# Optimization experiments

Measured on AMD Instinct MI355X. Metric: run time of the kernel, lower is better.

The kernel has to match this reference:

```python
import jax, jax.numpy as jnp
import numpy as np

DIMVEC = 196
POS_LABEL = 98
NBLABELS = 10
M = 128
UNIHIGH = 0.012
BATCH = 8192


def setup_inputs() -> dict:
    key = jax.random.key(0)
    ks = jax.random.split(key, 6)
    # input features: one 2-vector per site, normalized to unit norm (cos/sin style)
    x = jax.random.uniform(ks[0], (BATCH, DIMVEC, 2), dtype=jnp.float32)
    x = x / jnp.linalg.norm(x, axis=-1, keepdims=True)
    # MPS tensors, uniform(0, unihigh) as in the original construct_tensornetwork
    w0 = jax.random.uniform(ks[1], (2, M), dtype=jnp.float32) * UNIHIGH
    w_left = jax.random.uniform(ks[2], (POS_LABEL - 1, 2, M, M), dtype=jnp.float32) * UNIHIGH
    w_label = jax.random.uniform(ks[3], (2, M, M, NBLABELS), dtype=jnp.float32) * UNIHIGH
    w_right = jax.random.uniform(ks[4], (DIMVEC - 2 - POS_LABEL, 2, M, M), dtype=jnp.float32) * UNIHIGH
    w_end = jax.random.uniform(ks[5], (2, M), dtype=jnp.float32) * UNIHIGH
    return {"x": x, "w0": w0, "w_left": w_left, "w_label": w_label,
            "w_right": w_right, "w_end": w_end}


def reference(x, w0, w_left, w_label, w_right, w_end):
    b, d, _ = x.shape
    m = w0.shape[1]

    # left boundary: contract physical leg of site 0 -> [B, m]
    left = x[:, 0, :] @ w0

    # sweep sites 1 .. pos_label-1: left'[b,n] = sum_{p,mm} x[b,p] left[b,mm] W[p,mm,n]
    def lstep(carry, inp):
        W, xi = inp                       # W: [2,m,m], xi: [B,2]
        o = (xi[:, :, None] * carry[:, None, :]).reshape(b, 2 * m)  # [B, 2m]
        return o @ W.reshape(2 * m, m), None                        # GEMM B x 2m x m

    left, _ = jax.lax.scan(lstep, left,
                           (w_left, jnp.swapaxes(x[:, 1:POS_LABEL], 0, 1)))

    # right boundary: contract physical leg of last site -> [B, m]
    right = x[:, -1, :] @ w_end

    # sweep sites dimvec-2 .. pos_label+1 (reverse):
    # right'[b,mm] = sum_{p,n} x[b,p] right[b,n] W[p,mm,n]
    def rstep(carry, inp):
        W, xi = inp
        o = (xi[:, :, None] * carry[:, None, :]).reshape(b, 2 * m)  # [B, 2m]
        Wt = jnp.swapaxes(W, 1, 2).reshape(2 * m, m)                # [p,n,mm] -> [2m, m]
        return o @ Wt, None

    right, _ = jax.lax.scan(rstep, right,
                            (w_right, jnp.swapaxes(x[:, POS_LABEL + 1:d - 1], 0, 1)),
                            reverse=True)

    # label site: contract left bond first (small intermediate [B,2,m,L])
    xl = x[:, POS_LABEL, :]                                   # [B, 2]
    z = jnp.einsum('bm,pmnl->bpnl', left, w_label)             # [B,2,m,L]
    leftL = jnp.einsum('bpnl,bp->bnl', z, xl)                  # [B,m,L]

    # close the chain with the right environment -> [B, nblabels]
    return jnp.einsum('bnl,bn->bl', leftL, right)
```

## Files before the change

kernel.cpp:

```cpp
#include <hip/hip_runtime.h>

#define BATCH 8192
#define MDIM 128
#define NL 10
#define LSTEPS 97
#define RSTEPS 96
#define NSTEPS 193
#define DIM 196
#define POSL 98

typedef _Float16 half8 __attribute__((ext_vector_type(8)));
typedef float float16v __attribute__((ext_vector_type(16)));

#define BARRIER_LGKM() asm volatile("s_waitcnt lgkmcnt(0)\ns_barrier" ::: "memory")

#define MFMA16 __builtin_amdgcn_mfma_f32_32x32x16_f16

__global__ __launch_bounds__(256) void transpose_x(const float* __restrict__ x,
                                                   float2* __restrict__ xT) {
    __shared__ float tx[64][65];
    __shared__ float ty[64][65];
    int p0 = blockIdx.x * 32;
    int b0 = blockIdx.y * 64;
    int tid = threadIdx.x;

    int r = tid >> 2, q = tid & 3;
    const float* src = x + ((size_t)(b0 + r) * DIM + p0 + q * 8) * 2;
#pragma unroll
    for (int j = 0; j < 8; ++j) {
        int pp = q * 8 + j;
        if (p0 + pp < DIM) {
            float2 v = *(const float2*)(src + j * 2);
            tx[r][pp] = v.x;
            ty[r][pp] = v.y;
        }
    }
    __syncthreads();

    int pr = tid >> 3, cb = (tid & 7) * 8;
    if (p0 + pr < DIM) {
        float2* dst = xT + (size_t)(p0 + pr) * BATCH + b0 + cb;
#pragma unroll
        for (int j = 0; j < 8; ++j) {
            float2 v;
            v.x = tx[cb + j][pr];
            v.y = ty[cb + j][pr];
            dst[j] = v;
        }
    }
}

__global__ __launch_bounds__(256) void pack_w(const float* __restrict__ w_left,
                                              const float* __restrict__ w_right,
                                              _Float16* __restrict__ pw) {
    int g = blockIdx.x >> 2;
    int nt = blockIdx.x & 3;
    int tid = threadIdx.x;
    int l = tid & 63;
    int kq = tid >> 6;
    int hi = l >> 5;
    int n = nt * 32 + (l & 31);
#pragma unroll
    for (int p = 0; p < 4; ++p) {
        int kt = p * 4 + kq;
        int k0 = kt * 16 + hi * 8;
        half8 hv;
        if (g < LSTEPS) {
            const float* base = w_left + (size_t)g * 2 * MDIM * MDIM;
#pragma unroll
            for (int j = 0; j < 8; ++j)
                hv[j] = (_Float16)base[(size_t)(k0 + j) * MDIM + n];
        } else {
            int t = g - LSTEPS;
            int s = k0 >> 7;
            int a0 = k0 & 127;
            const float* row = w_right + (size_t)(RSTEPS - 1 - t) * 2 * MDIM * MDIM
                             + (size_t)s * MDIM * MDIM + (size_t)n * MDIM + a0;
#pragma unroll
            for (int j = 0; j < 8; ++j) hv[j] = (_Float16)row[j];
        }
        *(half8*)(pw + (size_t)(g * 64 + nt * 16 + kt) * 512 + l * 8) = hv;
    }
}

__global__ __launch_bounds__(256) void pack_label(const float* __restrict__ w_label,
                                                  _Float16* __restrict__ gp) {
    int ct = blockIdx.x;
    int tid = threadIdx.x;
    int l = tid & 63;
    int kq = tid >> 6;
    int hi = l >> 5;
    int outcol = ct * 32 + (l & 31);
    int n = outcol & 127;
    int lab = outcol >> 7;
#pragma unroll
    for (int p2 = 0; p2 < 4; ++p2) {
        int kt = p2 * 4 + kq;
        int k0 = kt * 16 + hi * 8;
        int p = k0 >> 7;
        int m0 = k0 & 127;
        half8 hv;
#pragma unroll
        for (int j = 0; j < 8; ++j)
            hv[j] = (_Float16)w_label[(((size_t)p * MDIM + m0 + j) * MDIM + n) * NL + lab];
        *(half8*)(gp + (size_t)(ct * 16 + kt) * 512 + l * 8) = hv;
    }
}


#define LD16(dst, p, ofs) \
    asm volatile("global_load_dwordx4 %0, %1, off offset:" ofs : "=v"(dst) : "v"(p))

#define ISSUE_A(DST, PN) do {                                  \
    const char* _p0 = (PN);                                    \
    LD16(DST[0],  _p0, "0");                                   \
    LD16(DST[1],  _p0, "1024");                                \
    LD16(DST[2],  _p0, "2048");                                \
    LD16(DST[3],  _p0, "3072");                                \
    const char* _p1 = _p0 + 4096;                              \
    LD16(DST[4],  _p1, "0");                                   \
    LD16(DST[5],  _p1, "1024");                                \
    LD16(DST[6],  _p1, "2048");                                \
    LD16(DST[7],  _p1, "3072");                                \
    const char* _p2 = _p0 + 8192;                              \
    LD16(DST[8],  _p2, "0");                                   \
    LD16(DST[9],  _p2, "1024");                                \
    LD16(DST[10], _p2, "2048");                                \
    LD16(DST[11], _p2, "3072");                                \
    const char* _p3 = _p0 + 12288;                             \
    LD16(DST[12], _p3, "0");                                   \
    LD16(DST[13], _p3, "1024");                                \
    LD16(DST[14], _p3, "2048");                                \
    LD16(DST[15], _p3, "3072");                                \
} while (0)

#define WAIT_A16() do {                                        \
    asm volatile("s_waitcnt vmcnt(16)" ::: "memory");          \
    __builtin_amdgcn_sched_barrier(0);                         \
} while (0)

#define WAIT_A0() do {                                         \
    asm volatile("s_waitcnt vmcnt(0)" ::: "memory");           \
    __builtin_amdgcn_sched_barrier(0);                         \
} while (0)

#define CHAIN_MFMA_BLOCK(AF, SRC)                                            \
    half8 bf0[8], bf1[8];                                                    \
    _Pragma("unroll")                                                        \
    for (int q = 0; q < 8; ++q) {                                            \
        int nb = q * 2 + hi;                                                 \
        int phys = nb ^ (bl & 15);                                           \
        bf0[q] = *(const half8*)&cbuf[SRC][bl * 128 + phys * 8];             \
        bf1[q] = *(const half8*)&cbuf[SRC][(bl + 32) * 128 + phys * 8];      \
    }                                                                        \
    float16v a00 = {}, a01 = {}, a10 = {}, a11 = {};                         \
    _Pragma("unroll")                                                        \
    for (int kt = 0; kt < 8; ++kt) {                                         \
        a00 = MFMA16(AF[kt], bf0[kt], a00, 0, 0, 0);                         \
        a10 = MFMA16(AF[kt], bf1[kt], a10, 0, 0, 0);                         \
        a01 = MFMA16(AF[kt + 8], bf0[kt], a01, 0, 0, 0);                     \
        a11 = MFMA16(AF[kt + 8], bf1[kt], a11, 0, 0, 0);                     \
    }

#define EPI_RG(DST, XC, A_LO, A_HI, ROWOFF)                                  \
    _Pragma("unroll")                                                        \
    for (int rq = 0; rq < 4; ++rq) {                                         \
        int nb = nt * 4 + rq;                                                \
        int phys = nb ^ (bl & 15);                                           \
        union { _Float16 h[4]; uint2 u; } t;                                 \
        _Pragma("unroll")                                                    \
        for (int r = 0; r < 4; ++r)                                          \
            t.h[r] = (_Float16)((XC).x * A_LO[rq * 4 + r]                    \
                              + (XC).y * A_HI[rq * 4 + r]);                  \
        *(uint2*)&cbuf[DST][(bl + ROWOFF) * 128 + phys * 8 + hi * 4] = t.u;  \
    }

#define FINAL_STORE()                                                        \
    _Pragma("unroll")                                                        \
    for (int r = 0; r < 16; ++r) {                                           \
        int n = nt * 32 + (r & 3) + 8 * (r >> 2) + 4 * hi;                   \
        outT[(size_t)n * BATCH + bbase + bl] = xc0.x * a00[r] + xc0.y * a01[r]; \
        outT[(size_t)n * BATCH + bbase + 32 + bl] = xc1.x * a10[r] + xc1.y * a11[r]; \
    }

__global__ __launch_bounds__(256, 1) void chain_mfma(
        const float2* __restrict__ xT, const float* __restrict__ w0,
        const float* __restrict__ w_end, const _Float16* __restrict__ pw,
        float* __restrict__ leftT, float* __restrict__ rightT) {
    __shared__ _Float16 cbuf[2][64 * 128];
    __shared__ float2 xbuf[98][64];

    int bid = blockIdx.x;
    bool is_left = bid < 128;
    int bbase = (is_left ? bid : bid - 128) * 64;
    int tid = threadIdx.x;
    int l = tid & 63;
    int nt = tid >> 6;
    int bl = l & 31;
    int hi = l >> 5;

    int nsteps = is_left ? LSTEPS : RSTEPS;
    int gbase = is_left ? 0 : LSTEPS;
    int pbase = is_left ? 0 : 98;
    float* outT = is_left ? leftT : rightT;

    for (int i = tid; i < 98 * 64; i += 256) {
        int pos = i >> 6, b = i & 63;
        xbuf[pos][b] = xT[(size_t)(pbase + pos) * BATCH + bbase + b];
    }
    __syncthreads();

    {
        const float* wst = is_left ? w0 : w_end;
        int b = tid >> 2;
        float2 xv0 = xbuf[is_left ? 0 : 97][b];
#pragma unroll
        for (int h = 0; h < 4; ++h) {
            int nb = (tid & 3) * 4 + h;
            half8 hv;
#pragma unroll
            for (int j = 0; j < 8; ++j) {
                int n = nb * 8 + j;
                hv[j] = (_Float16)(xv0.x * wst[n] + xv0.y * wst[MDIM + n]);
            }
            int phys = nb ^ (b & 15);
            *(half8*)&cbuf[0][b * 128 + phys * 8] = hv;
        }
    }

    const char* pwb = (const char*)pw + (size_t)(gbase * 64 + nt * 16) * 1024
                    + (size_t)l * 16;

    __syncthreads();

    half8 A0[16], A1[16];
    ISSUE_A(A0, pwb);

    int npairs = nsteps >> 1;
    bool oddtail = nsteps & 1;
    int last = nsteps - 1;

#pragma unroll 1
    for (int sp = 0; sp < npairs; ++sp) {
        int s0 = 2 * sp;
        {
            ISSUE_A(A1, pwb + (size_t)(s0 + 1) * 65536);
            WAIT_A16();
            int xi = is_left ? (1 + s0) : (96 - s0);
            float2 xc0 = xbuf[xi][bl];
            float2 xc1 = xbuf[xi][32 + bl];
            CHAIN_MFMA_BLOCK(A0, 0)
            EPI_RG(1, xc0, a00, a01, 0)
            EPI_RG(1, xc1, a10, a11, 32)
            BARRIER_LGKM();
        }
        {
            int s1 = s0 + 1;
            int pf = (s0 + 2 <= last) ? (s0 + 2) : last;
            ISSUE_A(A0, pwb + (size_t)pf * 65536);
            WAIT_A16();
            int xi = is_left ? (1 + s1) : (96 - s1);
            float2 xc0 = xbuf[xi][bl];
            float2 xc1 = xbuf[xi][32 + bl];
            CHAIN_MFMA_BLOCK(A1, 1)
            if (s1 == last) {
                FINAL_STORE()
            } else {
                EPI_RG(0, xc0, a00, a01, 0)
                EPI_RG(0, xc1, a10, a11, 32)
                BARRIER_LGKM();
            }
        }
    }

    if (oddtail) {
        WAIT_A0();
        int xi = 1 + last;
        float2 xc0 = xbuf[xi][bl];
        float2 xc1 = xbuf[xi][32 + bl];
        CHAIN_MFMA_BLOCK(A0, 0)
        FINAL_STORE()
    }
}

__global__ __launch_bounds__(256, 2) void label_mfma(
        const float2* __restrict__ xT, const _Float16* __restrict__ gp,
        const float* __restrict__ leftT, const float* __restrict__ rightT,
        float* __restrict__ out) {
    __shared__ _Float16 R[32 * 256];
    __shared__ float pl[4][32][5];
    __shared__ float xl_s[32][2];

    int bx = blockIdx.x;
    int bbase = blockIdx.y * 32;
    int tid = threadIdx.x;
    int l = tid & 63, nt = tid >> 6, bl = l & 31, hi = l >> 5;

    if (tid < 32) {
        const float2 v = xT[(size_t)POSL * BATCH + bbase + tid];
        xl_s[tid][0] = v.x; xl_s[tid][1] = v.y;
    }
    __syncthreads();

#pragma unroll
    for (int q = 0; q < 4; ++q) {
        int id = tid + q * 256;
        int m = id >> 3;
        int b4 = (id & 7) * 4;
        float4 v = *(const float4*)&leftT[(size_t)m * BATCH + bbase + b4];
        float vv[4] = {v.x, v.y, v.z, v.w};
#pragma unroll
        for (int bi = 0; bi < 4; ++bi) {
            int b = b4 + bi;
            int kb0 = m >> 3;
            int ph0 = (kb0 & 16) | ((kb0 ^ b) & 15);
            R[b * 256 + ph0 * 8 + (m & 7)] = (_Float16)(xl_s[b][0] * vv[bi]);
            int kb1 = kb0 + 16;
            int ph1 = (kb1 & 16) | ((kb1 ^ b) & 15);
            R[b * 256 + ph1 * 8 + (m & 7)] = (_Float16)(xl_s[b][1] * vv[bi]);
        }
    }

    float rv[16];
#pragma unroll
    for (int r = 0; r < 16; ++r) {
        int n = nt * 32 + (r & 3) + 8 * (r >> 2) + 4 * hi;
        rv[r] = rightT[(size_t)n * BATCH + bbase + bl];
    }
    __syncthreads();

    half8 rf[16];
#pragma unroll
    for (int kt = 0; kt < 16; ++kt) {
        int kb = kt * 2 + hi;
        int ph = (kb & 16) | ((kb ^ bl) & 15);
        rf[kt] = *(const half8*)&R[bl * 256 + ph * 8];
    }

    int l0 = bx * 5;
    float outv[5];
#pragma unroll
    for (int li = 0; li < 5; ++li) {
        int ct = (l0 + li) * 4 + nt;
        float16v acc = {};
#pragma unroll
        for (int kt = 0; kt < 16; ++kt) {
            half8 a = *(const half8*)(gp + (size_t)(ct * 16 + kt) * 512 + l * 8);
            acc = __builtin_amdgcn_mfma_f32_32x32x16_f16(a, rf[kt], acc, 0, 0, 0);
        }
        float p = 0.f;
#pragma unroll
        for (int r = 0; r < 16; ++r) p += acc[r] * rv[r];
        p += __shfl_xor(p, 32, 64);
        outv[li] = p;
    }
    if (hi == 0) {
#pragma unroll
        for (int li = 0; li < 5; ++li) pl[nt][bl][li] = outv[li];
    }
    __syncthreads();
    if (tid < 160) {
        int b = tid / 5, li = tid % 5;
        out[(size_t)(bbase + b) * NL + l0 + li] =
            pl[0][b][li] + pl[1][b][li] + pl[2][b][li] + pl[3][b][li];
    }
}

extern "C" void kernel_launch(void* const* d_in, const int* in_sizes, int n_in,
                              void* d_out, int out_size, void* d_ws, size_t ws_size,
                              hipStream_t stream) {
    const float* x       = (const float*)d_in[0];
    const float* w0      = (const float*)d_in[1];
    const float* w_left  = (const float*)d_in[2];
    const float* w_label = (const float*)d_in[3];
    const float* w_right = (const float*)d_in[4];
    const float* w_end   = (const float*)d_in[5];

    _Float16* pw = (_Float16*)d_ws;
    _Float16* gp = pw + (size_t)NSTEPS * 64 * 512;
    float* leftT  = (float*)(gp + (size_t)40 * 16 * 512);
    float* rightT = leftT + (size_t)MDIM * BATCH;
    float2* xT    = (float2*)(rightT + (size_t)MDIM * BATCH);

    transpose_x<<<dim3((DIM + 31) / 32, BATCH / 64), 256, 0, stream>>>(x, xT);
    pack_w<<<dim3(NSTEPS * 4), 256, 0, stream>>>(w_left, w_right, pw);
    pack_label<<<dim3(40), 256, 0, stream>>>(w_label, gp);
    chain_mfma<<<dim3(256), 256, 0, stream>>>(xT, w0, w_end, pw, leftT, rightT);
    label_mfma<<<dim3(2, BATCH / 32), 256, 0, stream>>>(xT, gp, leftT, rightT,
                                                        (float*)d_out);
}
```

Before: 241.8 us.

## Split chain kernel batch rows across two wave groups with 512-thread blocks

```diff
diff --git a/kernel.cpp b/kernel.cpp
--- a/kernel.cpp
+++ b/kernel.cpp
@@ -145,24 +145,21 @@
 } while (0)
 
 #define CHAIN_MFMA_BLOCK(AF, SRC)                                            \
-    half8 bf0[8], bf1[8];                                                    \
+    half8 bf[8];                                                             \
     _Pragma("unroll")                                                        \
     for (int q = 0; q < 8; ++q) {                                            \
         int nb = q * 2 + hi;                                                 \
         int phys = nb ^ (bl & 15);                                           \
-        bf0[q] = *(const half8*)&cbuf[SRC][bl * 128 + phys * 8];             \
-        bf1[q] = *(const half8*)&cbuf[SRC][(bl + 32) * 128 + phys * 8];      \
+        bf[q] = *(const half8*)&cbuf[SRC][row * 128 + phys * 8];             \
     }                                                                        \
-    float16v a00 = {}, a01 = {}, a10 = {}, a11 = {};                         \
+    float16v a0 = {}, a1 = {};                                               \
     _Pragma("unroll")                                                        \
     for (int kt = 0; kt < 8; ++kt) {                                         \
-        a00 = MFMA16(AF[kt], bf0[kt], a00, 0, 0, 0);                         \
-        a10 = MFMA16(AF[kt], bf1[kt], a10, 0, 0, 0);                         \
-        a01 = MFMA16(AF[kt + 8], bf0[kt], a01, 0, 0, 0);                     \
-        a11 = MFMA16(AF[kt + 8], bf1[kt], a11, 0, 0, 0);                     \
-    }
-
-#define EPI_RG(DST, XC, A_LO, A_HI, ROWOFF)                                  \
+        a0 = MFMA16(AF[kt], bf[kt], a0, 0, 0, 0);                            \
+        a1 = MFMA16(AF[kt + 8], bf[kt], a1, 0, 0, 0);                        \
+    }
+
+#define EPI_RG(DST, XC)                                                      \
     _Pragma("unroll")                                                        \
     for (int rq = 0; rq < 4; ++rq) {                                         \
         int nb = nt * 4 + rq;                                                \
@@ -170,20 +167,19 @@
         union { _Float16 h[4]; uint2 u; } t;                                 \
         _Pragma("unroll")                                                    \
         for (int r = 0; r < 4; ++r)                                          \
-            t.h[r] = (_Float16)((XC).x * A_LO[rq * 4 + r]                    \
-                              + (XC).y * A_HI[rq * 4 + r]);                  \
-        *(uint2*)&cbuf[DST][(bl + ROWOFF) * 128 + phys * 8 + hi * 4] = t.u;  \
-    }
-
-#define FINAL_STORE()                                                        \
+            t.h[r] = (_Float16)((XC).x * a0[rq * 4 + r]                      \
+                              + (XC).y * a1[rq * 4 + r]);                    \
+        *(uint2*)&cbuf[DST][row * 128 + phys * 8 + hi * 4] = t.u;            \
+    }
+
+#define FINAL_STORE(XC)                                                      \
     _Pragma("unroll")                                                        \
     for (int r = 0; r < 16; ++r) {                                           \
         int n = nt * 32 + (r & 3) + 8 * (r >> 2) + 4 * hi;                   \
-        outT[(size_t)n * BATCH + bbase + bl] = xc0.x * a00[r] + xc0.y * a01[r]; \
-        outT[(size_t)n * BATCH + bbase + 32 + bl] = xc1.x * a10[r] + xc1.y * a11[r]; \
-    }
-
-__global__ __launch_bounds__(256, 1) void chain_mfma(
+        outT[(size_t)n * BATCH + bbase + row] = (XC).x * a0[r] + (XC).y * a1[r]; \
+    }
+
+__global__ __launch_bounds__(512, 2) void chain_mfma(
         const float2* __restrict__ xT, const float* __restrict__ w0,
         const float* __restrict__ w_end, const _Float16* __restrict__ pw,
         float* __restrict__ leftT, float* __restrict__ rightT) {
@@ -195,16 +191,19 @@
     int bbase = (is_left ? bid : bid - 128) * 64;
     int tid = threadIdx.x;
     int l = tid & 63;
-    int nt = tid >> 6;
+    int w = tid >> 6;
+    int nt = w & 3;
+    int rg = w >> 2;
     int bl = l & 31;
     int hi = l >> 5;
+    int row = rg * 32 + bl;
 
     int nsteps = is_left ? LSTEPS : RSTEPS;
     int gbase = is_left ? 0 : LSTEPS;
     int pbase = is_left ? 0 : 98;
     float* outT = is_left ? leftT : rightT;
 
-    for (int i = tid; i < 98 * 64; i += 256) {
+    for (int i = tid; i < 98 * 64; i += 512) {
         int pos = i >> 6, b = i & 63;
         xbuf[pos][b] = xT[(size_t)(pbase + pos) * BATCH + bbase + b];
     }
@@ -212,11 +211,11 @@
 
     {
         const float* wst = is_left ? w0 : w_end;
-        int b = tid >> 2;
+        int b = tid >> 3;
         float2 xv0 = xbuf[is_left ? 0 : 97][b];
 #pragma unroll
-        for (int h = 0; h < 4; ++h) {
-            int nb = (tid & 3) * 4 + h;
+        for (int h = 0; h < 2; ++h) {
+            int nb = (tid & 7) * 2 + h;
             half8 hv;
 #pragma unroll
             for (int j = 0; j < 8; ++j) {
@@ -247,11 +246,9 @@
             ISSUE_A(A1, pwb + (size_t)(s0 + 1) * 65536);
             WAIT_A16();
             int xi = is_left ? (1 + s0) : (96 - s0);
-            float2 xc0 = xbuf[xi][bl];
-            float2 xc1 = xbuf[xi][32 + bl];
+            float2 xc = xbuf[xi][row];
             CHAIN_MFMA_BLOCK(A0, 0)
-            EPI_RG(1, xc0, a00, a01, 0)
-            EPI_RG(1, xc1, a10, a11, 32)
+            EPI_RG(1, xc)
             BARRIER_LGKM();
         }
         {
@@ -260,14 +257,12 @@
             ISSUE_A(A0, pwb + (size_t)pf * 65536);
             WAIT_A16();
             int xi = is_left ? (1 + s1) : (96 - s1);
-            float2 xc0 = xbuf[xi][bl];
-            float2 xc1 = xbuf[xi][32 + bl];
+            float2 xc = xbuf[xi][row];
             CHAIN_MFMA_BLOCK(A1, 1)
             if (s1 == last) {
-                FINAL_STORE()
+                FINAL_STORE(xc)
             } else {
-                EPI_RG(0, xc0, a00, a01, 0)
-                EPI_RG(0, xc1, a10, a11, 32)
+                EPI_RG(0, xc)
                 BARRIER_LGKM();
             }
         }
@@ -275,11 +270,9 @@
 
     if (oddtail) {
         WAIT_A0();
-        int xi = 1 + last;
-        float2 xc0 = xbuf[xi][bl];
-        float2 xc1 = xbuf[xi][32 + bl];
+        float2 xc = xbuf[1 + last][row];
         CHAIN_MFMA_BLOCK(A0, 0)
-        FINAL_STORE()
+        FINAL_STORE(xc)
     }
 }
 
@@ -385,7 +378,7 @@
     transpose_x<<<dim3((DIM + 31) / 32, BATCH / 64), 256, 0, stream>>>(x, xT);
     pack_w<<<dim3(NSTEPS * 4), 256, 0, stream>>>(w_left, w_right, pw);
     pack_label<<<dim3(40), 256, 0, stream>>>(w_label, gp);
-    chain_mfma<<<dim3(256), 256, 0, stream>>>(xT, w0, w_end, pw, leftT, rightT);
+    chain_mfma<<<dim3(256), 512, 0, stream>>>(xT, w0, w_end, pw, leftT, rightT);
     label_mfma<<<dim3(2, BATCH / 32), 256, 0, stream>>>(xT, gp, leftT, rightT,
                                                         (float*)d_out);
 }
```

Measured after the change: 253.9 us. +5.0%, slower.
